# Kernel tuning notes

Measured on AMD Instinct MI355X. Metric: run time of the kernel, lower is better.

The kernel has to match this reference:

```python
import jax, jax.numpy as jnp
import numpy as np

TEMPERATURE = 0.07
EPS = 1e-12  # F.normalize eps


def _l2_normalize(x):
    # matches torch F.normalize(dim=1): x / max(||x||, eps)
    n = jnp.linalg.norm(x, axis=1, keepdims=True)
    return x / jnp.maximum(n, EPS)


def setup_inputs() -> dict:
    key = jax.random.key(0)
    k1, k2 = jax.random.split(key)
    N, Z = 4096, 256
    z1 = jax.random.normal(k1, (N, Z), dtype=jnp.float32)
    z2 = jax.random.normal(k2, (N, Z), dtype=jnp.float32)
    return {"z1": z1, "z2": z2}


def reference(z1, z2):
    N = z1.shape[0]
    z1n = _l2_normalize(z1)
    z2n = _l2_normalize(z2)
    reps = jnp.concatenate([z1n, z2n], axis=0)          # [2N, Z]
    sim = reps @ reps.T                                  # cosine sim (rows unit-norm)
    # positives: sim[i, i+N] for i<N and sim[i, i-N] for i>=N
    pos = jnp.concatenate([jnp.diagonal(sim, offset=N),
                           jnp.diagonal(sim, offset=-N)])  # [2N]
    # The row logits are {positive} U {all sims except self and positive},
    # i.e. all entries except the self-similarity diagonal.
    inv_t = 1.0 / TEMPERATURE
    twoN = 2 * N
    diag_mask = jnp.eye(twoN, dtype=bool)
    logits = jnp.where(diag_mask, -jnp.inf, sim * inv_t)   # [2N, 2N]
    lse = jax.nn.logsumexp(logits, axis=1)                 # [2N]
    # cross_entropy with label at the positive: -pos/T + lse, sum / 2N
    loss = jnp.mean(lse - pos * inv_t)
    return loss
```

## Files before the change

### kernel.cpp

```cpp
#include <hip/hip_runtime.h>
#include <hip/hip_bf16.h>

#define N_ROWS 4096
#define TWO_N  8192
#define ZDIM   256
#define INV_T  (1.0f/0.07f)
#define EXP_SCALE (INV_T * 1.44269504088896340736f)

typedef __attribute__((ext_vector_type(8))) short bf16x8;
typedef __attribute__((ext_vector_type(4))) float f32x4;

__device__ __forceinline__ void async_load16(const void* g, void* lds_uniform_base) {
  __builtin_amdgcn_global_load_lds(
      (const __attribute__((address_space(1))) void*)g,
      (__attribute__((address_space(3))) void*)lds_uniform_base, 16, 0, 0);
}

__global__ __launch_bounds__(256) void normalize_kernel(
    const float* __restrict__ z1, const float* __restrict__ z2,
    __hip_bfloat16* __restrict__ reps, float* __restrict__ pos,
    float* __restrict__ rowsum) {
  const int b = blockIdx.x;
  const int t = threadIdx.x;
  const float x1 = z1[b * ZDIM + t];
  const float x2 = z2[b * ZDIM + t];
  float s1 = x1 * x1, s2 = x2 * x2, s3 = x1 * x2;
  #pragma unroll
  for (int m = 1; m < 64; m <<= 1) {
    s1 += __shfl_xor(s1, m, 64);
    s2 += __shfl_xor(s2, m, 64);
    s3 += __shfl_xor(s3, m, 64);
  }
  __shared__ float red[3][4];
  const int w = t >> 6, l = t & 63;
  if (l == 0) { red[0][w] = s1; red[1][w] = s2; red[2][w] = s3; }
  __syncthreads();
  const float n1 = red[0][0] + red[0][1] + red[0][2] + red[0][3];
  const float n2 = red[1][0] + red[1][1] + red[1][2] + red[1][3];
  const float dt = red[2][0] + red[2][1] + red[2][2] + red[2][3];
  const float inv1 = 1.0f / fmaxf(sqrtf(n1), 1e-12f);
  const float inv2 = 1.0f / fmaxf(sqrtf(n2), 1e-12f);
  reps[b * ZDIM + t]            = __float2bfloat16(x1 * inv1);
  reps[(b + N_ROWS) * ZDIM + t] = __float2bfloat16(x2 * inv2);
  if (t == 0) {
    pos[b] = dt * inv1 * inv2;
    rowsum[b] = 0.0f;
    rowsum[b + N_ROWS] = 0.0f;
  }
}

__global__ __launch_bounds__(256, 2) void simsum_kernel(
    const __hip_bfloat16* __restrict__ reps, float* __restrict__ rowsum) {
  __shared__ __align__(16) __hip_bfloat16 Alds[128 * 256];
  __shared__ __align__(16) __hip_bfloat16 Blds[128 * 64];

  const int tid  = threadIdx.x;
  const int lane = tid & 63;
  const int wave = tid >> 6;
  const int wm = wave >> 1, wn = wave & 1;
  const int quad = lane >> 4;
  const int l16  = lane & 15;
  const int rowBase  = blockIdx.x * 128;
  const int colChunk = blockIdx.y * 1024;
  const char* gbase = (const char*)reps;

  #pragma unroll
  for (int p = 0; p < 16; ++p) {
    const int cbase = p * 256 + (wave << 6);
    const int c = cbase + lane;
    const int row = c >> 5;
    const int ch = (c & 31) ^ (row & 7);
    const int gofs = ((rowBase + row) * ZDIM + ch * 8) * 2;
    async_load16(gbase + gofs, (char*)Alds + cbase * 16);
  }

  float rowpart[16];
  #pragma unroll
  for (int i = 0; i < 16; ++i) rowpart[i] = 0.0f;

  const f32x4 zero4 = {0.0f, 0.0f, 0.0f, 0.0f};

  for (int ct = 0; ct < 8; ++ct) {
    const int colBase = colChunk + ct * 128;
    f32x4 acc[4][4];
    #pragma unroll
    for (int mi = 0; mi < 4; ++mi)
      #pragma unroll
      for (int ni = 0; ni < 4; ++ni) acc[mi][ni] = zero4;

    for (int kc = 0; kc < 4; ++kc) {
      #pragma unroll
      for (int p = 0; p < 4; ++p) {
        const int cbase = p * 256 + (wave << 6);
        const int c = cbase + lane;
        const int row = c >> 3;
        const int ch = (c & 7) ^ (row & 7);
        const int gofs = ((colBase + row) * ZDIM + kc * 64 + ch * 8) * 2;
        async_load16(gbase + gofs, (char*)Blds + cbase * 16);
      }
      __syncthreads();

      #pragma unroll
      for (int kk2 = 0; kk2 < 2; ++kk2) {
        bf16x8 afrag[4], bfrag[4];
        #pragma unroll
        for (int mi = 0; mi < 4; ++mi) {
          const int m = wm * 64 + mi * 16 + l16;
          const int ch = kc * 8 + kk2 * 4 + quad;
          afrag[mi] = *(const bf16x8*)((const char*)Alds + (m * 32 + (ch ^ (m & 7))) * 16);
        }
        #pragma unroll
        for (int ni = 0; ni < 4; ++ni) {
          const int n = wn * 64 + ni * 16 + l16;
          const int ch = kk2 * 4 + quad;
          bfrag[ni] = *(const bf16x8*)((const char*)Blds + (n * 8 + (ch ^ (n & 7))) * 16);
        }
        #pragma unroll
        for (int mi = 0; mi < 4; ++mi)
          #pragma unroll
          for (int ni = 0; ni < 4; ++ni)
            acc[mi][ni] = __builtin_amdgcn_mfma_f32_16x16x32_bf16(
                afrag[mi], bfrag[ni], acc[mi][ni], 0, 0, 0);
      }
      __syncthreads();
    }

    #pragma unroll
    for (int mi = 0; mi < 4; ++mi) {
      #pragma unroll
      for (int r = 0; r < 4; ++r) {
        const int grow = rowBase + wm * 64 + mi * 16 + quad * 4 + r;
        float s = 0.0f;
        #pragma unroll
        for (int ni = 0; ni < 4; ++ni) {
          const int gcol = colBase + wn * 64 + ni * 16 + l16;
          const float v = acc[mi][ni][r];
          const float e = exp2f((v - 1.0f) * EXP_SCALE);
          if (grow != gcol) s += e;
        }
        rowpart[mi * 4 + r] += s;
      }
    }
  }

  #pragma unroll
  for (int i = 0; i < 16; ++i) {
    float v = rowpart[i];
    v += __shfl_xor(v, 1, 64);
    v += __shfl_xor(v, 2, 64);
    v += __shfl_xor(v, 4, 64);
    v += __shfl_xor(v, 8, 64);
    rowpart[i] = v;
  }
  if (l16 == 0) {
    #pragma unroll
    for (int mi = 0; mi < 4; ++mi)
      #pragma unroll
      for (int r = 0; r < 4; ++r)
        atomicAdd(&rowsum[rowBase + wm * 64 + mi * 16 + quad * 4 + r],
                  rowpart[mi * 4 + r]);
  }
}

__global__ __launch_bounds__(1024) void loss_kernel(
    const float* __restrict__ rowsum, const float* __restrict__ pos,
    float* __restrict__ out) {
  const int t = threadIdx.x;
  float slog = 0.0f;
  for (int i = t; i < TWO_N; i += 1024) slog += logf(rowsum[i]);
  float spos = 0.0f;
  for (int i = t; i < N_ROWS; i += 1024) spos += pos[i];
  #pragma unroll
  for (int m = 1; m < 64; m <<= 1) {
    slog += __shfl_xor(slog, m, 64);
    spos += __shfl_xor(spos, m, 64);
  }
  __shared__ float rl[16], rp[16];
  const int w = t >> 6, l = t & 63;
  if (l == 0) { rl[w] = slog; rp[w] = spos; }
  __syncthreads();
  if (t == 0) {
    float tl = 0.0f, tp = 0.0f;
    #pragma unroll
    for (int i = 0; i < 16; ++i) { tl += rl[i]; tp += rp[i]; }
    out[0] = INV_T + tl / (float)TWO_N - tp * INV_T / (float)N_ROWS;
  }
}

extern "C" void kernel_launch(void* const* d_in, const int* in_sizes, int n_in,
                              void* d_out, int out_size, void* d_ws, size_t ws_size,
                              hipStream_t stream) {
  const float* z1 = (const float*)d_in[0];
  const float* z2 = (const float*)d_in[1];
  __hip_bfloat16* reps = (__hip_bfloat16*)d_ws;
  float* rowsum = (float*)((char*)d_ws + (size_t)TWO_N * ZDIM * 2);
  float* pos = rowsum + TWO_N;

  normalize_kernel<<<N_ROWS, 256, 0, stream>>>(z1, z2, reps, pos, rowsum);
  simsum_kernel<<<dim3(64, 8), 256, 0, stream>>>(reps, rowsum);
  loss_kernel<<<1, 1024, 0, stream>>>(rowsum, pos, (float*)d_out);
}
```

Before: 111.7 us.

## Exploit symmetry of similarity matrix and fuse final loss into simsum kernel

Since the similarity matrix is symmetric, each block now computes only about half of the tiles: a cyclic offset schedule covers each unordered tile pair once. Each off-diagonal tile adds its exp values to both the row sums and, via atomics, the column sums. The diagonal tile reuses the A tile in LDS and skips the B loads. The separate loss kernel is removed, and the last block to finish, found through an atomic counter, computes the log-sum and the final loss, saving a launch at the cost of extra column atomics.

```diff
diff --git a/kernel.cpp b/kernel.cpp
--- a/kernel.cpp
+++ b/kernel.cpp
@@ -6,6 +6,7 @@
 #define ZDIM   256
 #define INV_T  (1.0f/0.07f)
 #define EXP_SCALE (INV_T * 1.44269504088896340736f)
+#define GRID_BLOCKS 512
 
 typedef __attribute__((ext_vector_type(8))) short bf16x8;
 typedef __attribute__((ext_vector_type(4))) float f32x4;
@@ -19,7 +20,7 @@
 __global__ __launch_bounds__(256) void normalize_kernel(
     const float* __restrict__ z1, const float* __restrict__ z2,
     __hip_bfloat16* __restrict__ reps, float* __restrict__ pos,
-    float* __restrict__ rowsum) {
+    float* __restrict__ rowsum, int* __restrict__ counter) {
   const int b = blockIdx.x;
   const int t = threadIdx.x;
   const float x1 = z1[b * ZDIM + t];
@@ -46,11 +47,14 @@
     pos[b] = dt * inv1 * inv2;
     rowsum[b] = 0.0f;
     rowsum[b + N_ROWS] = 0.0f;
+    if (b == 0) counter[0] = 0;
   }
 }
 
 __global__ __launch_bounds__(256, 2) void simsum_kernel(
-    const __hip_bfloat16* __restrict__ reps, float* __restrict__ rowsum) {
+    const __hip_bfloat16* __restrict__ reps, float* __restrict__ rowsum,
+    const float* __restrict__ pos, int* __restrict__ counter,
+    float* __restrict__ out) {
   __shared__ __align__(16) __hip_bfloat16 Alds[128 * 256];
   __shared__ __align__(16) __hip_bfloat16 Blds[128 * 64];
 
@@ -60,8 +64,9 @@
   const int wm = wave >> 1, wn = wave & 1;
   const int quad = lane >> 4;
   const int l16  = lane & 15;
-  const int rowBase  = blockIdx.x * 128;
-  const int colChunk = blockIdx.y * 1024;
+  const int itile = blockIdx.x;
+  const int chunk = blockIdx.y;
+  const int rowBase = itile * 128;
   const char* gbase = (const char*)reps;
 
   #pragma unroll
@@ -73,6 +78,12 @@
     const int gofs = ((rowBase + row) * ZDIM + ch * 8) * 2;
     async_load16(gbase + gofs, (char*)Alds + cbase * 16);
   }
+  __syncthreads();
+
+  int dlist[5];
+  int nd = 0;
+  for (int q = 0; q < 4; ++q) dlist[nd++] = 4 * chunk + q;
+  if (chunk == 0 && itile < 32) dlist[nd++] = 32;
 
   float rowpart[16];
   #pragma unroll
@@ -80,8 +91,12 @@
 
   const f32x4 zero4 = {0.0f, 0.0f, 0.0f, 0.0f};
 
-  for (int ct = 0; ct < 8; ++ct) {
-    const int colBase = colChunk + ct * 128;
+  for (int td = 0; td < nd; ++td) {
+    const int d = dlist[td];
+    const int jtile = (itile + d) & 63;
+    const int colBase = jtile * 128;
+    const bool diag = (d == 0);
+
     f32x4 acc[4][4];
     #pragma unroll
     for (int mi = 0; mi < 4; ++mi)
@@ -89,16 +104,18 @@
       for (int ni = 0; ni < 4; ++ni) acc[mi][ni] = zero4;
 
     for (int kc = 0; kc < 4; ++kc) {
-      #pragma unroll
-      for (int p = 0; p < 4; ++p) {
-        const int cbase = p * 256 + (wave << 6);
-        const int c = cbase + lane;
-        const int row = c >> 3;
-        const int ch = (c & 7) ^ (row & 7);
-        const int gofs = ((colBase + row) * ZDIM + kc * 64 + ch * 8) * 2;
-        async_load16(gbase + gofs, (char*)Blds + cbase * 16);
-      }
-      __syncthreads();
+      if (!diag) {
+        #pragma unroll
+        for (int p = 0; p < 4; ++p) {
+          const int cbase = p * 256 + (wave << 6);
+          const int c = cbase + lane;
+          const int row = c >> 3;
+          const int ch = (c & 7) ^ (row & 7);
+          const int gofs = ((colBase + row) * ZDIM + kc * 64 + ch * 8) * 2;
+          async_load16(gbase + gofs, (char*)Blds + cbase * 16);
+        }
+        __syncthreads();
+      }
 
       #pragma unroll
       for (int kk2 = 0; kk2 < 2; ++kk2) {
@@ -112,8 +129,13 @@
         #pragma unroll
         for (int ni = 0; ni < 4; ++ni) {
           const int n = wn * 64 + ni * 16 + l16;
-          const int ch = kk2 * 4 + quad;
-          bfrag[ni] = *(const bf16x8*)((const char*)Blds + (n * 8 + (ch ^ (n & 7))) * 16);
+          if (diag) {
+            const int ch = kc * 8 + kk2 * 4 + quad;
+            bfrag[ni] = *(const bf16x8*)((const char*)Alds + (n * 32 + (ch ^ (n & 7))) * 16);
+          } else {
+            const int ch = kk2 * 4 + quad;
+            bfrag[ni] = *(const bf16x8*)((const char*)Blds + (n * 8 + (ch ^ (n & 7))) * 16);
+          }
         }
         #pragma unroll
         for (int mi = 0; mi < 4; ++mi)
@@ -122,9 +144,10 @@
             acc[mi][ni] = __builtin_amdgcn_mfma_f32_16x16x32_bf16(
                 afrag[mi], bfrag[ni], acc[mi][ni], 0, 0, 0);
       }
-      __syncthreads();
-    }
-
+      if (!diag) __syncthreads();
+    }
+
+    float colpart[4] = {0.0f, 0.0f, 0.0f, 0.0f};
     #pragma unroll
     for (int mi = 0; mi < 4; ++mi) {
       #pragma unroll
@@ -136,9 +159,20 @@
           const int gcol = colBase + wn * 64 + ni * 16 + l16;
           const float v = acc[mi][ni][r];
           const float e = exp2f((v - 1.0f) * EXP_SCALE);
-          if (grow != gcol) s += e;
+          if (!diag || grow != gcol) s += e;
+          colpart[ni] += e;
         }
         rowpart[mi * 4 + r] += s;
+      }
+    }
+    if (!diag) {
+      #pragma unroll
+      for (int ni = 0; ni < 4; ++ni) {
+        float v = colpart[ni];
+        v += __shfl_xor(v, 16, 64);
+        v += __shfl_xor(v, 32, 64);
+        if (quad == 0)
+          atomicAdd(&rowsum[colBase + wn * 64 + ni * 16 + l16], v);
       }
     }
   }
@@ -160,30 +194,39 @@
         atomicAdd(&rowsum[rowBase + wm * 64 + mi * 16 + quad * 4 + r],
                   rowpart[mi * 4 + r]);
   }
-}
-
-__global__ __launch_bounds__(1024) void loss_kernel(
-    const float* __restrict__ rowsum, const float* __restrict__ pos,
-    float* __restrict__ out) {
-  const int t = threadIdx.x;
-  float slog = 0.0f;
-  for (int i = t; i < TWO_N; i += 1024) slog += logf(rowsum[i]);
-  float spos = 0.0f;
-  for (int i = t; i < N_ROWS; i += 1024) spos += pos[i];
-  #pragma unroll
-  for (int m = 1; m < 64; m <<= 1) {
-    slog += __shfl_xor(slog, m, 64);
-    spos += __shfl_xor(spos, m, 64);
-  }
-  __shared__ float rl[16], rp[16];
-  const int w = t >> 6, l = t & 63;
-  if (l == 0) { rl[w] = slog; rp[w] = spos; }
-  __syncthreads();
-  if (t == 0) {
-    float tl = 0.0f, tp = 0.0f;
-    #pragma unroll
-    for (int i = 0; i < 16; ++i) { tl += rl[i]; tp += rp[i]; }
-    out[0] = INV_T + tl / (float)TWO_N - tp * INV_T / (float)N_ROWS;
+
+  __threadfence();
+  __syncthreads();
+  int* flag = (int*)Blds;
+  if (tid == 0) {
+    const int old = __hip_atomic_fetch_add(counter, 1, __ATOMIC_ACQ_REL,
+                                           __HIP_MEMORY_SCOPE_AGENT);
+    flag[0] = (old == GRID_BLOCKS - 1) ? 1 : 0;
+  }
+  __syncthreads();
+  if (flag[0]) {
+    __threadfence();
+    float slog = 0.0f;
+    for (int r = tid; r < TWO_N; r += 256) {
+      const float rs = __hip_atomic_load(&rowsum[r], __ATOMIC_RELAXED,
+                                         __HIP_MEMORY_SCOPE_AGENT);
+      slog += logf(rs);
+    }
+    float spos = 0.0f;
+    for (int r = tid; r < N_ROWS; r += 256) spos += pos[r];
+    #pragma unroll
+    for (int m = 1; m < 64; m <<= 1) {
+      slog += __shfl_xor(slog, m, 64);
+      spos += __shfl_xor(spos, m, 64);
+    }
+    float* red = (float*)Blds + 8;
+    if (lane == 0) { red[wave] = slog; red[4 + wave] = spos; }
+    __syncthreads();
+    if (tid == 0) {
+      const float tl = red[0] + red[1] + red[2] + red[3];
+      const float tp = red[4] + red[5] + red[6] + red[7];
+      out[0] = INV_T + tl / (float)TWO_N - tp * INV_T / (float)N_ROWS;
+    }
   }
 }
 
@@ -195,8 +238,9 @@
   __hip_bfloat16* reps = (__hip_bfloat16*)d_ws;
   float* rowsum = (float*)((char*)d_ws + (size_t)TWO_N * ZDIM * 2);
   float* pos = rowsum + TWO_N;
-
-  normalize_kernel<<<N_ROWS, 256, 0, stream>>>(z1, z2, reps, pos, rowsum);
-  simsum_kernel<<<dim3(64, 8), 256, 0, stream>>>(reps, rowsum);
-  loss_kernel<<<1, 1024, 0, stream>>>(rowsum, pos, (float*)d_out);
-}
+  int* counter = (int*)(pos + N_ROWS);
+
+  normalize_kernel<<<N_ROWS, 256, 0, stream>>>(z1, z2, reps, pos, rowsum, counter);
+  simsum_kernel<<<dim3(64, 8), 256, 0, stream>>>(reps, rowsum, pos, counter,
+                                                 (float*)d_out);
+}
```

New measurement: 137.7 us. +23.3%, slower.
